# Performance work log

Hardware: AMD Instinct MI355X
Metric: run time of the kernel (lower is better)

Reference implementation:

```python
import jax, jax.numpy as jnp
import numpy as np

NUM_EMBEDDINGS = 1024
EMBEDDING_DIM = 256
BETA = 0.25


def setup_inputs() -> dict:
    key = jax.random.key(0)
    k1, k2 = jax.random.split(key)
    x = jax.random.normal(k1, (32, 256, 32, 32), dtype=jnp.float32)
    # nn.Embedding weight init: uniform(-1/K, 1/K)
    lim = 1.0 / NUM_EMBEDDINGS
    emb_weight = jax.random.uniform(k2, (NUM_EMBEDDINGS, EMBEDDING_DIM),
                                    dtype=jnp.float32, minval=-lim, maxval=lim)
    return {"x": x, "emb_weight": emb_weight}


def reference(x, emb_weight):
    b, c, h, w = x.shape
    # [b, h, w, c] -> [N, c]
    x_flat = jnp.transpose(x, (0, 2, 3, 1)).reshape(-1, c)
    distances = (jnp.sum(x_flat * x_flat, axis=1, keepdims=True)
                 - 2.0 * jnp.einsum('nc,kc->nk', x_flat, emb_weight)
                 + jnp.sum(emb_weight * emb_weight, axis=1))
    indices = jnp.argmin(distances, axis=1)  # [N]
    quantized = emb_weight[indices].reshape(b, h, w, c).transpose(0, 3, 1, 2)
    sg = jax.lax.stop_gradient
    commitment_loss = jnp.mean((sg(quantized) - x) ** 2)
    embedding_loss = jnp.mean((quantized - sg(x)) ** 2)
    loss = commitment_loss + BETA * embedding_loss
    return quantized, loss, indices.reshape(b, h, w)
```

## Files before the change

kernel.cpp:

```cpp
#include <hip/hip_runtime.h>

#define LOSS_OFF 8388608
#define IDX_OFF  8388609

#define WS_SEE   0
#define WS_SXX   4096
#define WS_KEY   135168
#define WS_CNT   397312
#define WS_LOSS  397320
#define WS_WL    397328
#define WS_EP    528448

#define FLT_BIG  3.402823466e+38f
#define MARGIN   1.0e-4f

typedef __attribute__((ext_vector_type(8))) short  short8v;
typedef __attribute__((ext_vector_type(4))) float  float4v;

#define GLD16(gp, lp) __builtin_amdgcn_global_load_lds( \
    (const __attribute__((address_space(1))) unsigned int*)(gp), \
    (__attribute__((address_space(3))) unsigned int*)(lp), 16, 0, 0)

__device__ __forceinline__ float np_sumsq256(const float* __restrict__ p, int stride) {
    float s[2];
#pragma unroll
    for (int half = 0; half < 2; half++) {
        const float* a = p + half * 128 * stride;
        float r[8];
#pragma unroll
        for (int l = 0; l < 8; l++) {
            float v = a[l * stride];
            float sq = v * v;
            asm volatile("" : "+v"(sq));
            r[l] = sq;
        }
#pragma unroll
        for (int i = 8; i < 128; i += 8) {
#pragma unroll
            for (int l = 0; l < 8; l++) {
                float v = a[(i + l) * stride];
                float sq = v * v;
                asm volatile("" : "+v"(sq));
                r[l] = r[l] + sq;
            }
        }
        s[half] = ((r[0] + r[1]) + (r[2] + r[3])) + ((r[4] + r[5]) + (r[6] + r[7]));
    }
    return s[0] + s[1];
}

__device__ __forceinline__ unsigned int f32_sortable(float m) {
    unsigned int u = __float_as_uint(m);
    return u ^ (((unsigned int)((int)u >> 31)) | 0x80000000u);
}
__device__ __forceinline__ float f32_unsortable(unsigned int s) {
    const unsigned int u = (s >> 31) ? (s ^ 0x80000000u) : ~s;
    return __uint_as_float(u);
}

__device__ __forceinline__ unsigned short f2bf(float f) {
    unsigned int u = __float_as_uint(f);
    return (unsigned short)((u + 0x7fffu + ((u >> 16) & 1u)) >> 16);
}
__device__ __forceinline__ float bf2f(unsigned short h) {
    return __uint_as_float(((unsigned int)h) << 16);
}

__global__ __launch_bounds__(256) void k_prep(const float* __restrict__ emb,
                                              unsigned short* __restrict__ ebP,
                                              float* __restrict__ see,
                                              float* __restrict__ eT,
                                              int* __restrict__ cnt,
                                              double* __restrict__ loss) {
    const int t = threadIdx.x, bb = blockIdx.x;
    if (bb < 256) {
        const int idx = bb * 256 + t;
        const int l  = idx & 63;
        const int ph = (idx >> 6) & 1;
        const int ct = (idx >> 7) & 7;
        const int cc = (idx >> 10) & 7;
        const int cg = (idx >> 13) & 7;
        const int row = cg * 128 + ct * 16 + (l & 15);
        const int col = cc * 32 + (l >> 4) * 8;
        const float* src = emb + (size_t)row * 256 + col;
        uint4 out;
        unsigned short* op = (unsigned short*)&out;
#pragma unroll
        for (int i = 0; i < 8; i++) {
            const float v = src[i];
            const unsigned short h = f2bf(v);
            op[i] = ph ? f2bf(v - bf2f(h)) : h;
        }
        *(uint4*)(ebP + (size_t)idx * 8) = out;
    } else if (bb < 260) {
        const int k = (bb - 256) * 256 + t;
        see[k] = np_sumsq256(emb + (size_t)k * 256, 1);
        if (k == 0) { *cnt = 0; *loss = 0.0; }
    } else {
        __shared__ float T[256][17];
        const int k0 = (bb - 260) << 4;
        const int kr = t >> 4, cs = (t & 15) << 4;
#pragma unroll
        for (int j = 0; j < 4; j++) {
            const float4 v = *(const float4*)(emb + (size_t)(k0 + kr) * 256 + cs + j * 4);
            T[cs + j * 4 + 0][kr] = v.x;
            T[cs + j * 4 + 1][kr] = v.y;
            T[cs + j * 4 + 2][kr] = v.z;
            T[cs + j * 4 + 3][kr] = v.w;
        }
        __syncthreads();
        float* dst = eT + (size_t)t * 1024 + k0;
#pragma unroll
        for (int j = 0; j < 4; j++) {
            float4 v;
            v.x = T[t][j * 4 + 0]; v.y = T[t][j * 4 + 1];
            v.z = T[t][j * 4 + 2]; v.w = T[t][j * 4 + 3];
            *(float4*)(dst + j * 4) = v;
        }
    }
}

#define LOADB(buf, ccv, cth) do {                                              \
    _Pragma("unroll")                                                          \
    for (int q = 0; q < 4; q++) {                                              \
        const int ctq = (cth) * 4 + q;                                         \
        const size_t bbq = ((((size_t)codeg * 8 + (ccv)) * 8 + ctq) * 2) * 512 \
                           + (size_t)l * 8;                                    \
        buf[2 * q]     = *(const short8v*)(ebP + bbq);                         \
        buf[2 * q + 1] = *(const short8v*)(ebP + bbq + 512);                   \
    }                                                                          \
} while (0)

#define MFMA_CT(ctv, BH, BL) do {                                              \
    _Pragma("unroll")                                                          \
    for (int at = 0; at < 4; at++) {                                           \
        acc[at][ctv] = __builtin_amdgcn_mfma_f32_16x16x32_bf16(ah[at], BH, acc[at][ctv], 0, 0, 0); \
        acc[at][ctv] = __builtin_amdgcn_mfma_f32_16x16x32_bf16(ah[at], BL, acc[at][ctv], 0, 0, 0); \
        acc[at][ctv] = __builtin_amdgcn_mfma_f32_16x16x32_bf16(al[at], BH, acc[at][ctv], 0, 0, 0); \
    }                                                                          \
} while (0)

__global__ __launch_bounds__(512, 2) void k1_mfma(
        const float* __restrict__ x,
        const unsigned short* __restrict__ ebP,
        const float* __restrict__ see_g,
        float* __restrict__ sxx_g,
        unsigned long long* __restrict__ key,
        double* __restrict__ loss,
        int* __restrict__ cnt, int* __restrict__ wl) {
    __shared__ char smem[131072];
    unsigned long long* lk1 = (unsigned long long*)smem;
    float*              lg2 = (float*)(smem + 4096);
    float* xstage = (float*)smem;
    char*  frag   = smem + 65536;

    const int t = threadIdx.x;
    const int w = t >> 6, l = t & 63;
    const int codeg = w;
    const int lrow = l >> 4, lcol = l & 15;
    const int rb = blockIdx.x;
    const int n0 = rb * 64;
    const int b  = rb >> 4;
    const int hw0 = (rb & 15) << 6;

    {
        const char* xbyte = (const char*)x + ((size_t)b * 262144 + hw0) * 4;
#pragma unroll
        for (int i = 0; i < 8; i++) {
            const int cbase = i * 32 + w * 4;
            const char* src = xbyte + (size_t)(cbase + (l >> 4)) * 4096 + (size_t)(l & 15) * 16;
            GLD16(src, smem + cbase * 256);
        }
    }
    __syncthreads();

#pragma unroll
    for (int ii = 0; ii < 4; ii++) {
        const int pi  = ii * 512 + t;
        const int pcc = pi >> 8;
        const int pat = (pi >> 6) & 3;
        const int pl  = pi & 63;
        const int prow = pat * 16 + (pl & 15);
        const int pc0  = pcc * 32 + (pl >> 4) * 8;
        uint4 hp, lp;
        unsigned short* hpp = (unsigned short*)&hp;
        unsigned short* lpp = (unsigned short*)&lp;
#pragma unroll
        for (int i = 0; i < 8; i++) {
            const float v = xstage[(pc0 + i) * 64 + prow];
            const unsigned short h = f2bf(v);
            hpp[i] = h;
            lpp[i] = f2bf(v - bf2f(h));
        }
        char* dst = frag + pcc * 8192 + pat * 2048 + pl * 16;
        *(uint4*)dst = hp;
        *(uint4*)(dst + 1024) = lp;
    }
    float sx_reg = 0.f;
    if (t < 64) {
        sx_reg = np_sumsq256(xstage + t, 64);
        sxx_g[n0 + t] = sx_reg;
    }
    __syncthreads();

    float4v acc[4][8];
#pragma unroll
    for (int at = 0; at < 4; at++)
#pragma unroll
        for (int ct = 0; ct < 8; ct++) acc[at][ct] = (float4v){0.f, 0.f, 0.f, 0.f};

    short8v b0[8], b1[8];
    LOADB(b0, 0, 0);
    for (int cc = 0; cc < 8; cc++) {
        short8v ah[4], al[4];
#pragma unroll
        for (int at = 0; at < 4; at++) {
            const int off = cc * 8192 + at * 2048 + l * 16;
            ah[at] = *(const short8v*)(frag + off);
            al[at] = *(const short8v*)(frag + off + 1024);
        }
        LOADB(b1, cc, 1);
        MFMA_CT(0, b0[0], b0[1]);
        MFMA_CT(1, b0[2], b0[3]);
        MFMA_CT(2, b0[4], b0[5]);
        MFMA_CT(3, b0[6], b0[7]);
        if (cc < 7) LOADB(b0, cc + 1, 0);
        MFMA_CT(4, b1[0], b1[1]);
        MFMA_CT(5, b1[2], b1[3]);
        MFMA_CT(6, b1[4], b1[5]);
        MFMA_CT(7, b1[6], b1[7]);
    }

    float sv[8];
#pragma unroll
    for (int ct = 0; ct < 8; ct++) sv[ct] = see_g[codeg * 128 + ct * 16 + lcol];

#pragma unroll
    for (int at = 0; at < 4; at++) {
#pragma unroll
        for (int j = 0; j < 4; j++) {
            unsigned long long K1 = ~0ull; float G1 = FLT_BIG, G2 = FLT_BIG;
#pragma unroll
            for (int ct = 0; ct < 8; ct++) {
                const float g = fmaf(-2.f, acc[at][ct][j], sv[ct]);
                const int k = codeg * 128 + ct * 16 + lcol;
                const unsigned long long pk =
                    ((unsigned long long)f32_sortable(g) << 32) | (unsigned int)k;
                if (pk < K1) { G2 = G1; K1 = pk; G1 = g; }
                else         { G2 = fminf(G2, g); }
            }
#pragma unroll
            for (int m = 1; m < 16; m <<= 1) {
                const unsigned long long oK = __shfl_xor(K1, m, 64);
                const float oG2 = __shfl_xor(G2, m, 64);
                const float oG1 = f32_unsortable((unsigned int)(oK >> 32));
                if (oK < K1) { G2 = fminf(oG2, G1); K1 = oK; G1 = oG1; }
                else         { G2 = fminf(G2, oG1); }
            }
            const int rloc = at * 16 + lrow * 4 + j;
            if (lcol == 0) { lk1[rloc * 8 + codeg] = K1; lg2[rloc * 8 + codeg] = G2; }
        }
    }
    __syncthreads();
    if (t < 64) {
        unsigned long long K1 = ~0ull; float G1 = FLT_BIG, G2 = FLT_BIG;
        for (int cg = 0; cg < 8; cg++) {
            const unsigned long long oK = lk1[t * 8 + cg];
            const float oG2 = lg2[t * 8 + cg];
            const float oG1 = f32_unsortable((unsigned int)(oK >> 32));
            if (oK < K1) { G2 = fminf(oG2, G1); K1 = oK; G1 = oG1; }
            else         { G2 = fminf(G2, oG1); }
        }
        const int n = n0 + t;
        if (G2 - G1 > MARGIN) { key[n] = K1; }
        else { key[n] = ~0ull; wl[atomicAdd(cnt, 1)] = n; }
        float part = sx_reg + G1;
#pragma unroll
        for (int m = 1; m < 64; m <<= 1) part += __shfl_xor(part, m, 64);
        if (t == 0) atomicAdd(loss, (double)part);
    }
}

__global__ __launch_bounds__(256) void k2r(const float* __restrict__ x,
                                           const float* __restrict__ eT,
                                           const float* __restrict__ see,
                                           const float* __restrict__ sxx,
                                           unsigned long long* __restrict__ key,
                                           const int* __restrict__ cnt,
                                           const int* __restrict__ wl) {
    __shared__ float xs[8][264];
    const int t = threadIdx.x;
    const int total = *cnt;
    for (int base = blockIdx.x * 8; base < total; base += 128 * 8) {
        int nrow[8]; float sx8[8];
#pragma unroll
        for (int r = 0; r < 8; r++) {
            int idx = base + r; if (idx >= total) idx = total - 1;
            const int n = wl[idx];
            nrow[r] = n; sx8[r] = sxx[n];
        }
        __syncthreads();
#pragma unroll
        for (int r = 0; r < 8; r++) {
            const int n = nrow[r];
            xs[r][t] = x[(size_t)(n >> 10) * 262144 + (size_t)t * 1024 + (n & 1023)];
        }
        __syncthreads();
        float d[8][4];
#pragma unroll
        for (int r = 0; r < 8; r++)
#pragma unroll
            for (int j = 0; j < 4; j++) d[r][j] = 0.f;
#pragma unroll 4
        for (int c = 0; c < 256; c++) {
            float ev[4];
#pragma unroll
            for (int j = 0; j < 4; j++) ev[j] = eT[(size_t)c * 1024 + t + 256 * j];
#pragma unroll
            for (int r = 0; r < 8; r++) {
                const float xv = xs[r][c];
                d[r][0] = fmaf(xv, ev[0], d[r][0]);
                d[r][1] = fmaf(xv, ev[1], d[r][1]);
                d[r][2] = fmaf(xv, ev[2], d[r][2]);
                d[r][3] = fmaf(xv, ev[3], d[r][3]);
            }
        }
#pragma unroll
        for (int r = 0; r < 8; r++) {
            unsigned long long best = ~0ull;
#pragma unroll
            for (int j = 0; j < 4; j++) {
                const float q = fmaf(-2.f, d[r][j], sx8[r]) + see[t + 256 * j];
                const unsigned long long pk =
                    ((unsigned long long)f32_sortable(q) << 32) | (unsigned int)(t + 256 * j);
                best = pk < best ? pk : best;
            }
            atomicMin(&key[nrow[r]], best);
        }
    }
}

__global__ __launch_bounds__(256) void k3_out(const float* __restrict__ emb,
                                              const unsigned long long* __restrict__ key,
                                              const double* __restrict__ loss,
                                              float* __restrict__ dout) {
    __shared__ float elds[32][257];
    __shared__ int   idxs[32];
    const int t  = threadIdx.x;
    const int bh = blockIdx.x;
    const int b = bh >> 5, h = bh & 31;
    if (t < 32) idxs[t] = (int)(key[(bh << 5) + t] & 0xffffffffull);
    __syncthreads();
    for (int r = 0; r < 32; r++) elds[r][t] = emb[(size_t)idxs[r] * 256 + t];
    __syncthreads();
    const int w = t & 31, cg = t >> 5;
    const size_t base = (size_t)b * 262144 + (size_t)(h * 32 + w);
#pragma unroll 4
    for (int s = 0; s < 32; s++) {
        const int c = (cg << 5) + s;
        dout[base + (size_t)c * 1024] = elds[w][c];
    }
    if (t < 32) dout[IDX_OFF + (bh << 5) + t] = (float)idxs[t];
    if (bh == 0 && t == 0)
        dout[LOSS_OFF] = (float)(1.25 * (*loss) / 8388608.0);
}

extern "C" void kernel_launch(void* const* d_in, const int* in_sizes, int n_in,
                              void* d_out, int out_size, void* d_ws, size_t ws_size,
                              hipStream_t stream) {
    const float* x   = (const float*)d_in[0];
    const float* emb = (const float*)d_in[1];
    float* dout = (float*)d_out;
    char* ws = (char*)d_ws;
    float*  see  = (float*)(ws + WS_SEE);
    float*  sxx  = (float*)(ws + WS_SXX);
    unsigned long long* key = (unsigned long long*)(ws + WS_KEY);
    int*    cnt  = (int*)(ws + WS_CNT);
    double* loss = (double*)(ws + WS_LOSS);
    int*    wl   = (int*)(ws + WS_WL);
    unsigned short* ebP = (unsigned short*)(ws + WS_EP);
    float* eT = dout;

    k_prep <<<324,  256, 0, stream>>>(emb, ebP, see, eT, cnt, loss);
    k1_mfma<<<512,  512, 0, stream>>>(x, ebP, see, sxx, key, loss, cnt, wl);
    k2r    <<<128,  256, 0, stream>>>(x, eT, see, sxx, key, cnt, wl);
    k3_out <<<1024, 256, 0, stream>>>(emb, key, loss, dout);
}
```

Measured before the change: 178.7 us.

## Fuse near-tie exact fp32 recheck into MFMA kernel, drop separate k2r pass

Ambiguous rows, where the top-two distance gap falls below the margin, are now recomputed exactly in fp32 inside the MFMA kernel, reusing the x tile already staged in LDS. This replaces the global worklist, the atomic counter and the separate k2r launch. It removes one kernel launch and the global x re-gather. In exchange each flagged row is handled serially by the whole block with two block barriers per row, which can stall blocks that hold many near-ties and may raise LDS use enough to affect occupancy.

```diff
diff --git a/kernel.cpp b/kernel.cpp
--- a/kernel.cpp
+++ b/kernel.cpp
@@ -4,12 +4,9 @@
 #define IDX_OFF  8388609
 
 #define WS_SEE   0
-#define WS_SXX   4096
-#define WS_KEY   135168
-#define WS_CNT   397312
-#define WS_LOSS  397320
-#define WS_WL    397328
-#define WS_EP    528448
+#define WS_KEY   4096
+#define WS_LOSS  266240
+#define WS_EP    266248
 
 #define FLT_BIG  3.402823466e+38f
 #define MARGIN   1.0e-4f
@@ -70,7 +67,6 @@
                                               unsigned short* __restrict__ ebP,
                                               float* __restrict__ see,
                                               float* __restrict__ eT,
-                                              int* __restrict__ cnt,
                                               double* __restrict__ loss) {
     const int t = threadIdx.x, bb = blockIdx.x;
     if (bb < 256) {
@@ -95,7 +91,7 @@
     } else if (bb < 260) {
         const int k = (bb - 256) * 256 + t;
         see[k] = np_sumsq256(emb + (size_t)k * 256, 1);
-        if (k == 0) { *cnt = 0; *loss = 0.0; }
+        if (k == 0) { *loss = 0.0; }
     } else {
         __shared__ float T[256][17];
         const int k0 = (bb - 260) << 4;
@@ -144,15 +140,17 @@
         const float* __restrict__ x,
         const unsigned short* __restrict__ ebP,
         const float* __restrict__ see_g,
-        float* __restrict__ sxx_g,
+        const float* __restrict__ eT,
         unsigned long long* __restrict__ key,
-        double* __restrict__ loss,
-        int* __restrict__ cnt, int* __restrict__ wl) {
-    __shared__ char smem[131072];
-    unsigned long long* lk1 = (unsigned long long*)smem;
-    float*              lg2 = (float*)(smem + 4096);
+        double* __restrict__ loss) {
+    __shared__ char smem[132096];
     float* xstage = (float*)smem;
     char*  frag   = smem + 65536;
+    unsigned long long* lk1 = (unsigned long long*)frag;
+    float*              lg2 = (float*)(frag + 4096);
+    float*              sxs = (float*)(smem + 131072);
+    int*                flg = (int*)(smem + 131328);
+    unsigned long long* red8 = (unsigned long long*)(smem + 131584);
 
     const int t = threadIdx.x;
     const int w = t >> 6, l = t & 63;
@@ -199,7 +197,7 @@
     float sx_reg = 0.f;
     if (t < 64) {
         sx_reg = np_sumsq256(xstage + t, 64);
-        sxx_g[n0 + t] = sx_reg;
+        sxs[t] = sx_reg;
     }
     __syncthreads();
 
@@ -230,6 +228,7 @@
         MFMA_CT(6, b1[4], b1[5]);
         MFMA_CT(7, b1[6], b1[7]);
     }
+    __syncthreads();
 
     float sv[8];
 #pragma unroll
@@ -272,71 +271,46 @@
             else         { G2 = fminf(G2, oG1); }
         }
         const int n = n0 + t;
-        if (G2 - G1 > MARGIN) { key[n] = K1; }
-        else { key[n] = ~0ull; wl[atomicAdd(cnt, 1)] = n; }
+        const int flagged = (G2 - G1 <= MARGIN);
+        flg[t] = flagged;
+        if (!flagged) key[n] = K1;
         float part = sx_reg + G1;
 #pragma unroll
         for (int m = 1; m < 64; m <<= 1) part += __shfl_xor(part, m, 64);
         if (t == 0) atomicAdd(loss, (double)part);
     }
-}
-
-__global__ __launch_bounds__(256) void k2r(const float* __restrict__ x,
-                                           const float* __restrict__ eT,
-                                           const float* __restrict__ see,
-                                           const float* __restrict__ sxx,
-                                           unsigned long long* __restrict__ key,
-                                           const int* __restrict__ cnt,
-                                           const int* __restrict__ wl) {
-    __shared__ float xs[8][264];
-    const int t = threadIdx.x;
-    const int total = *cnt;
-    for (int base = blockIdx.x * 8; base < total; base += 128 * 8) {
-        int nrow[8]; float sx8[8];
-#pragma unroll
-        for (int r = 0; r < 8; r++) {
-            int idx = base + r; if (idx >= total) idx = total - 1;
-            const int n = wl[idx];
-            nrow[r] = n; sx8[r] = sxx[n];
-        }
-        __syncthreads();
-#pragma unroll
-        for (int r = 0; r < 8; r++) {
-            const int n = nrow[r];
-            xs[r][t] = x[(size_t)(n >> 10) * 262144 + (size_t)t * 1024 + (n & 1023)];
-        }
-        __syncthreads();
-        float d[8][4];
-#pragma unroll
-        for (int r = 0; r < 8; r++)
-#pragma unroll
-            for (int j = 0; j < 4; j++) d[r][j] = 0.f;
+    __syncthreads();
+
+    for (int r = 0; r < 64; r++) {
+        if (!flg[r]) continue;
+        const float sx = sxs[r];
+        float d0 = 0.f, d1 = 0.f;
 #pragma unroll 4
         for (int c = 0; c < 256; c++) {
-            float ev[4];
-#pragma unroll
-            for (int j = 0; j < 4; j++) ev[j] = eT[(size_t)c * 1024 + t + 256 * j];
-#pragma unroll
-            for (int r = 0; r < 8; r++) {
-                const float xv = xs[r][c];
-                d[r][0] = fmaf(xv, ev[0], d[r][0]);
-                d[r][1] = fmaf(xv, ev[1], d[r][1]);
-                d[r][2] = fmaf(xv, ev[2], d[r][2]);
-                d[r][3] = fmaf(xv, ev[3], d[r][3]);
-            }
-        }
-#pragma unroll
-        for (int r = 0; r < 8; r++) {
-            unsigned long long best = ~0ull;
-#pragma unroll
-            for (int j = 0; j < 4; j++) {
-                const float q = fmaf(-2.f, d[r][j], sx8[r]) + see[t + 256 * j];
-                const unsigned long long pk =
-                    ((unsigned long long)f32_sortable(q) << 32) | (unsigned int)(t + 256 * j);
-                best = pk < best ? pk : best;
-            }
-            atomicMin(&key[nrow[r]], best);
-        }
+            const float xv = xstage[c * 64 + r];
+            d0 = fmaf(xv, eT[(size_t)c * 1024 + t], d0);
+            d1 = fmaf(xv, eT[(size_t)c * 1024 + t + 512], d1);
+        }
+        const float q0 = fmaf(-2.f, d0, sx) + see_g[t];
+        const float q1 = fmaf(-2.f, d1, sx) + see_g[t + 512];
+        unsigned long long best =
+            ((unsigned long long)f32_sortable(q0) << 32) | (unsigned int)t;
+        const unsigned long long pk1 =
+            ((unsigned long long)f32_sortable(q1) << 32) | (unsigned int)(t + 512);
+        best = pk1 < best ? pk1 : best;
+#pragma unroll
+        for (int m = 1; m < 64; m <<= 1) {
+            const unsigned long long o = __shfl_xor(best, m, 64);
+            best = o < best ? o : best;
+        }
+        if (l == 0) red8[w] = best;
+        __syncthreads();
+        if (t == 0) {
+            unsigned long long mkey = red8[0];
+            for (int i = 1; i < 8; i++) mkey = red8[i] < mkey ? red8[i] : mkey;
+            key[n0 + r] = mkey;
+        }
+        __syncthreads();
     }
 }
 
@@ -373,16 +347,12 @@
     float* dout = (float*)d_out;
     char* ws = (char*)d_ws;
     float*  see  = (float*)(ws + WS_SEE);
-    float*  sxx  = (float*)(ws + WS_SXX);
     unsigned long long* key = (unsigned long long*)(ws + WS_KEY);
-    int*    cnt  = (int*)(ws + WS_CNT);
     double* loss = (double*)(ws + WS_LOSS);
-    int*    wl   = (int*)(ws + WS_WL);
     unsigned short* ebP = (unsigned short*)(ws + WS_EP);
     float* eT = dout;
 
-    k_prep <<<324,  256, 0, stream>>>(emb, ebP, see, eT, cnt, loss);
-    k1_mfma<<<512,  512, 0, stream>>>(x, ebP, see, sxx, key, loss, cnt, wl);
-    k2r    <<<128,  256, 0, stream>>>(x, eT, see, sxx, key, cnt, wl);
+    k_prep <<<324,  256, 0, stream>>>(emb, ebP, see, eT, loss);
+    k1_mfma<<<512,  512, 0, stream>>>(x, ebP, see, eT, key, loss);
     k3_out <<<1024, 256, 0, stream>>>(emb, key, loss, dout);
 }
```

Result: slower. 200.2 us (+12.0%).
